# Performance work log

Measured on AMD Instinct MI355X. Metric: run time of the kernel, lower is better.

Reference implementation:

```python
import jax, jax.numpy as jnp
import numpy as np

NB_HEAD = 8
SIZE_PER_HEAD = 64
MAX_LEN = 1024
D_IN = 512
BATCH = 8
NEG_BIG = 1e12  # matches the torch module's mask * 1000000000000.0


def setup_inputs() -> dict:
    key = jax.random.key(0)
    ks = jax.random.split(key, 6)
    return {
        "Q_seq": jax.random.normal(ks[0], (BATCH, MAX_LEN, D_IN), dtype=jnp.float32),
        "K_seq": jax.random.normal(ks[1], (BATCH, MAX_LEN, D_IN), dtype=jnp.float32),
        "V_seq": jax.random.normal(ks[2], (BATCH, MAX_LEN, D_IN), dtype=jnp.float32),
        "WQ": jax.random.normal(ks[3], (D_IN, NB_HEAD * SIZE_PER_HEAD), dtype=jnp.float32),
        "WK": jax.random.normal(ks[4], (D_IN, NB_HEAD * SIZE_PER_HEAD), dtype=jnp.float32),
        "WV": jax.random.normal(ks[5], (D_IN, NB_HEAD * SIZE_PER_HEAD), dtype=jnp.float32),
    }


def reference(Q_seq, K_seq, V_seq, WQ, WK, WV):
    B, L, _ = Q_seq.shape
    H, D = NB_HEAD, SIZE_PER_HEAD
    # QKV projections -> [B, H, L, D]
    q = (Q_seq @ WQ).reshape(B, L, H, D).transpose(0, 2, 1, 3)
    k = (K_seq @ WK).reshape(B, L, H, D).transpose(0, 2, 1, 3)
    v = (V_seq @ WV).reshape(B, L, H, D).transpose(0, 2, 1, 3)
    # scaled dot-product scores [B, H, Lq, Lk]
    scores = jnp.einsum("bhqd,bhkd->bhqk", q, k) / jnp.sqrt(jnp.float32(D))
    # causal mask: the torch Mask() subtracts 1e12 where key_idx > query_idx
    causal = jnp.triu(jnp.ones((L, L), dtype=scores.dtype), k=1)  # 1 where k > q
    scores = scores - causal[None, None, :, :] * NEG_BIG
    attn = jax.nn.softmax(scores, axis=-1)
    out = jnp.einsum("bhqk,bhkd->bhqd", attn, v)  # [B, H, L, D]
    return out.transpose(0, 2, 1, 3).reshape(B, L, H * D)
```

## Files before the change

kernel.cpp:

```cpp
#include <hip/hip_runtime.h>
#include <cstddef>

#define LEN    1024
#define DIN    512
#define NHEAD  8
#define HDIM   64
#define BATCH  8

typedef __attribute__((ext_vector_type(8))) short  short8;
typedef __attribute__((ext_vector_type(4))) float  f32x4;

#define MFMA16(a, b, c) __builtin_amdgcn_mfma_f32_16x16x32_bf16((a), (b), (c), 0, 0, 0)
#define PERM_HI 0x07060302u
#define PERM_LO 0x05040100u

__device__ __forceinline__ unsigned short bf_hi(float x) {
    unsigned u = __float_as_uint(x);
    return (unsigned short)((u + 0x7fffu + ((u >> 16) & 1u)) >> 16);
}
__device__ __forceinline__ void bf_split(float x, unsigned short& h, unsigned short& l) {
    unsigned u  = __float_as_uint(x);
    unsigned hu = (u + 0x7fffu + ((u >> 16) & 1u)) >> 16;
    h = (unsigned short)hu;
    l = bf_hi(x - __uint_as_float(hu << 16));
}
__device__ __forceinline__ void unpack4(uint4 u, ushort4& h, ushort4& l) {
    h = make_ushort4((unsigned short)(u.x >> 16), (unsigned short)(u.y >> 16),
                     (unsigned short)(u.z >> 16), (unsigned short)(u.w >> 16));
    l = make_ushort4((unsigned short)(u.x & 0xffff), (unsigned short)(u.y & 0xffff),
                     (unsigned short)(u.z & 0xffff), (unsigned short)(u.w & 0xffff));
}
__device__ __forceinline__ void unpack8(uint4 a, uint4 b, uint4& h, uint4& l) {
    h = make_uint4(__builtin_amdgcn_perm(a.y, a.x, PERM_HI),
                   __builtin_amdgcn_perm(a.w, a.z, PERM_HI),
                   __builtin_amdgcn_perm(b.y, b.x, PERM_HI),
                   __builtin_amdgcn_perm(b.w, b.z, PERM_HI));
    l = make_uint4(__builtin_amdgcn_perm(a.y, a.x, PERM_LO),
                   __builtin_amdgcn_perm(a.w, a.z, PERM_LO),
                   __builtin_amdgcn_perm(b.y, b.x, PERM_LO),
                   __builtin_amdgcn_perm(b.w, b.z, PERM_LO));
}

template<int CTRL>
__device__ __forceinline__ float dpp_mov(float x) {
    return __int_as_float(__builtin_amdgcn_update_dpp(
        0, __float_as_int(x), CTRL, 0xF, 0xF, true));
}
__device__ __forceinline__ float red16_max(float x) {
    x = fmaxf(x, dpp_mov<0xB1>(x));
    x = fmaxf(x, dpp_mov<0x4E>(x));
    x = fmaxf(x, dpp_mov<0x141>(x));
    x = fmaxf(x, dpp_mov<0x140>(x));
    return x;
}
__device__ __forceinline__ float red16_sum(float x) {
    x += dpp_mov<0xB1>(x);
    x += dpp_mov<0x4E>(x);
    x += dpp_mov<0x141>(x);
    x += dpp_mov<0x140>(x);
    return x;
}

__global__ __launch_bounds__(256)
void wprep(const float* __restrict__ WQ, const float* __restrict__ WK,
           const float* __restrict__ WV, unsigned short* __restrict__ wt)
{
    __shared__ float T[64][68];
    const int z = blockIdx.z;
    const float* W = (z == 0) ? WQ : (z == 1) ? WK : WV;
    unsigned short* Wth = wt + (size_t)z * 524288;
    unsigned short* Wtl = Wth + 262144;
    const int k0 = blockIdx.x * 64, n0 = blockIdx.y * 64;
    const int t = threadIdx.x;
    #pragma unroll
    for (int e = 0; e < 4; ++e) {
        int f = e * 256 + t, r = f >> 4, c4 = (f & 15) << 2;
        *(float4*)&T[r][c4] = *(const float4*)&W[(size_t)(k0 + r) * 512 + n0 + c4];
    }
    __syncthreads();
    #pragma unroll
    for (int e = 0; e < 4; ++e) {
        int f = e * 256 + t, nr = f >> 4, kc4 = (f & 15) << 2;
        ushort4 h, l;
        bf_split(T[kc4 + 0][nr], h.x, l.x);
        bf_split(T[kc4 + 1][nr], h.y, l.y);
        bf_split(T[kc4 + 2][nr], h.z, l.z);
        bf_split(T[kc4 + 3][nr], h.w, l.w);
        *(ushort4*)&Wth[(size_t)(n0 + nr) * 512 + k0 + kc4] = h;
        *(ushort4*)&Wtl[(size_t)(n0 + nr) * 512 + k0 + kc4] = l;
    }
}

#define PSTR 40

__global__ __launch_bounds__(256)
void proj_mfma(const float* __restrict__ Qin, const float* __restrict__ Kin,
               const float* __restrict__ Vin, const unsigned short* __restrict__ wt,
               unsigned int* __restrict__ qhl, unsigned int* __restrict__ khl,
               unsigned short* __restrict__ vh)
{
    __shared__ unsigned short Ah[128 * PSTR], Al[128 * PSTR],
                              Bh[128 * PSTR], Bl[128 * PSTR];
    const int z = blockIdx.z;
    const bool full = (z < 2);
    const float* X = (z == 0) ? Qin : (z == 1) ? Kin : Vin;
    const unsigned short* Wth = wt + (size_t)z * 524288;
    const unsigned short* Wtl = Wth + 262144;

    const int t = threadIdx.x, lane = t & 63, w = t >> 6;
    const int wm = w & 1, wn = w >> 1;
    const int m0 = blockIdx.x * 128, n0 = blockIdx.y * 128;
    const int lm = lane & 15, lq = lane >> 4;
    const int ar = t >> 1, ak = (t & 1) * 16;

    const float* Xp = X + (size_t)(m0 + ar) * 512 + ak;
    const unsigned short* Bph = Wth + (size_t)(n0 + ar) * 512 + ak;
    const unsigned short* Bpl = Wtl + (size_t)(n0 + ar) * 512 + ak;

    f32x4 acc[4][4];
    #pragma unroll
    for (int i = 0; i < 4; ++i)
        #pragma unroll
        for (int j = 0; j < 4; ++j) acc[i][j] = 0.f;

    float4 av[4];
    uint4 bh0, bh1, bl0, bl1;
    #pragma unroll
    for (int e = 0; e < 4; ++e) av[e] = *(const float4*)(Xp + e * 4);
    bh0 = *(const uint4*)(Bph);
    bh1 = *(const uint4*)(Bph + 8);
    if (full) { bl0 = *(const uint4*)(Bpl); bl1 = *(const uint4*)(Bpl + 8); }

    for (int k0 = 0; k0 < 512; k0 += 32) {
        __syncthreads();
        {
            const float* ff = (const float*)&av[0];
            uint hw[16];
            #pragma unroll
            for (int i = 0; i < 16; ++i) hw[i] = __float_as_uint(ff[i]) & 0xffff0000u;
            uint4 ahv  = make_uint4(__builtin_amdgcn_perm(hw[1],  hw[0],  PERM_HI),
                                    __builtin_amdgcn_perm(hw[3],  hw[2],  PERM_HI),
                                    __builtin_amdgcn_perm(hw[5],  hw[4],  PERM_HI),
                                    __builtin_amdgcn_perm(hw[7],  hw[6],  PERM_HI));
            uint4 ahv2 = make_uint4(__builtin_amdgcn_perm(hw[9],  hw[8],  PERM_HI),
                                    __builtin_amdgcn_perm(hw[11], hw[10], PERM_HI),
                                    __builtin_amdgcn_perm(hw[13], hw[12], PERM_HI),
                                    __builtin_amdgcn_perm(hw[15], hw[14], PERM_HI));
            *(uint4*)&Ah[ar * PSTR + ak]     = ahv;
            *(uint4*)&Ah[ar * PSTR + ak + 8] = ahv2;
            if (full) {
                uint lo[8];
                #pragma unroll
                for (int i = 0; i < 8; ++i) {
                    float r0 = ff[2*i]   - __uint_as_float(hw[2*i]);
                    float r1 = ff[2*i+1] - __uint_as_float(hw[2*i+1]);
                    lo[i] = ((uint)bf_hi(r1) << 16) | bf_hi(r0);
                }
                *(uint4*)&Al[ar * PSTR + ak]     = make_uint4(lo[0], lo[1], lo[2], lo[3]);
                *(uint4*)&Al[ar * PSTR + ak + 8] = make_uint4(lo[4], lo[5], lo[6], lo[7]);
            }
        }
        *(uint4*)&Bh[ar * PSTR + ak]     = bh0;
        *(uint4*)&Bh[ar * PSTR + ak + 8] = bh1;
        if (full) {
            *(uint4*)&Bl[ar * PSTR + ak]     = bl0;
            *(uint4*)&Bl[ar * PSTR + ak + 8] = bl1;
        }
        __syncthreads();

        if (k0 + 32 < 512) {
            #pragma unroll
            for (int e = 0; e < 4; ++e) av[e] = *(const float4*)(Xp + k0 + 32 + e * 4);
            bh0 = *(const uint4*)(Bph + k0 + 32);
            bh1 = *(const uint4*)(Bph + k0 + 40);
            if (full) {
                bl0 = *(const uint4*)(Bpl + k0 + 32);
                bl1 = *(const uint4*)(Bpl + k0 + 40);
            }
        }

        short8 a_h[4], a_l[4];
        #pragma unroll
        for (int mi = 0; mi < 4; ++mi) {
            int off = (wm * 64 + mi * 16 + lm) * PSTR + lq * 8;
            a_h[mi] = *(const short8*)&Ah[off];
            if (full) a_l[mi] = *(const short8*)&Al[off];
        }
        #pragma unroll
        for (int ni = 0; ni < 4; ++ni) {
            int off = (wn * 64 + ni * 16 + lm) * PSTR + lq * 8;
            short8 b_h = *(const short8*)&Bh[off];
            if (full) {
                short8 b_l = *(const short8*)&Bl[off];
                #pragma unroll
                for (int mi = 0; mi < 4; ++mi) {
                    acc[mi][ni] = MFMA16(a_l[mi], b_h, acc[mi][ni]);
                    acc[mi][ni] = MFMA16(a_h[mi], b_l, acc[mi][ni]);
                    acc[mi][ni] = MFMA16(a_h[mi], b_h, acc[mi][ni]);
                }
            } else {
                #pragma unroll
                for (int mi = 0; mi < 4; ++mi)
                    acc[mi][ni] = MFMA16(a_h[mi], b_h, acc[mi][ni]);
            }
        }
    }

    if (z < 2) {
        unsigned int* o = (z == 0) ? qhl : khl;
        const float sc = (z == 0) ? 0.18033688011112042f : 1.0f;
        #pragma unroll
        for (int mi = 0; mi < 4; ++mi)
            #pragma unroll
            for (int ni = 0; ni < 4; ++ni) {
                int n_abs = n0 + wn * 64 + ni * 16 + lm;
                int hd = n_abs >> 6, d = n_abs & 63;
                #pragma unroll
                for (int r = 0; r < 4; ++r) {
                    int m_abs = m0 + wm * 64 + mi * 16 + lq * 4 + r;
                    int b = m_abs >> 10, li = m_abs & 1023;
                    unsigned short hv, lv;
                    bf_split(acc[mi][ni][r] * sc, hv, lv);
                    o[(((size_t)b * NHEAD + hd) * LEN + li) * HDIM + d] =
                        ((unsigned)hv << 16) | lv;
                }
            }
    } else {
        #pragma unroll
        for (int mi = 0; mi < 4; ++mi) {
            int m_base = m0 + wm * 64 + mi * 16 + lq * 4;
            int b = m_base >> 10, l0 = m_base & 1023;
            #pragma unroll
            for (int ni = 0; ni < 4; ++ni) {
                int n_abs = n0 + wn * 64 + ni * 16 + lm;
                int hd = n_abs >> 6, d = n_abs & 63;
                ushort4 hv = make_ushort4(bf_hi(acc[mi][ni][0]), bf_hi(acc[mi][ni][1]),
                                          bf_hi(acc[mi][ni][2]), bf_hi(acc[mi][ni][3]));
                *(ushort4*)&vh[(((size_t)b * NHEAD + hd) * HDIM + d) * LEN + l0] = hv;
            }
        }
    }
}

__global__ __launch_bounds__(256)
void attn_mfma(const unsigned int* __restrict__ qhl, const unsigned int* __restrict__ khl,
               const unsigned short* __restrict__ vth, float* __restrict__ out)
{
    __shared__ unsigned short sm[18432];
    unsigned short* Kh  = sm;
    unsigned short* Kl  = sm + 4608;
    unsigned short* Pb  = sm;
    unsigned short* Vt  = sm + 9216;
    unsigned short* Qsh = sm;
    unsigned short* Qsl = sm + 9216;

    const int t = threadIdx.x, lane = t & 63, w = t >> 6;
    const int lm = lane & 15, lq = lane >> 4;
    const int bx = blockIdx.x;
    const int qt = 7 - (bx >> 6);
    const int bh = bx & 63;
    const size_t base = (size_t)bh * LEN * HDIM;
    const unsigned int*   qb = qhl + base;
    const unsigned int*   kb = khl + base;
    const unsigned short* vb = vth + base;
    const int Q0  = qt * 128;
    const int Q0w = Q0 + w * 32;

    #pragma unroll
    for (int e = 0; e < 8; ++e) {
        int f = e * 256 + t, r = f >> 4, c4 = (f & 15) << 2;
        uint4 u = *(const uint4*)&qb[(size_t)(Q0 + r) * 64 + c4];
        ushort4 h, l;
        unpack4(u, h, l);
        *(ushort4*)&Qsh[r * 72 + c4] = h;
        *(ushort4*)&Qsl[r * 72 + c4] = l;
    }
    __syncthreads();
    short8 qfh[2][2], qfl[2][2];
    #pragma unroll
    for (int mi = 0; mi < 2; ++mi)
        #pragma unroll
        for (int ks = 0; ks < 2; ++ks) {
            int off = (w * 32 + mi * 16 + lm) * 72 + ks * 32 + lq * 8;
            qfh[mi][ks] = *(const short8*)&Qsh[off];
            qfl[mi][ks] = *(const short8*)&Qsl[off];
        }

    float m_i[2][4], l_i[2][4];
    f32x4 oacc[2][4];
    #pragma unroll
    for (int mi = 0; mi < 2; ++mi)
        #pragma unroll
        for (int r = 0; r < 4; ++r) { m_i[mi][r] = -1e30f; l_i[mi][r] = 0.f; }
    #pragma unroll
    for (int mi = 0; mi < 2; ++mi)
        #pragma unroll
        for (int nd = 0; nd < 4; ++nd) oacc[mi][nd] = 0.f;

    const int kr = t >> 2, kq = t & 3;
    const int vd_ = t >> 3, vs8 = (t & 7) << 3;

    uint4 kreg[4], vreg[2];
    #pragma unroll
    for (int e = 0; e < 4; ++e)
        kreg[e] = *(const uint4*)&kb[(size_t)kr * 64 + kq * 16 + e * 4];
    #pragma unroll
    for (int e = 0; e < 2; ++e)
        vreg[e] = *(const uint4*)&vb[(size_t)(e * 32 + vd_) * LEN + vs8];

    const int jend = 2 * qt + 1;
    for (int jb = 0; jb <= jend; ++jb) {
        __syncthreads();
        {
            uint4 h0, l0, h1, l1;
            unpack8(kreg[0], kreg[1], h0, l0);
            unpack8(kreg[2], kreg[3], h1, l1);
            int ko = kr * 72 + kq * 16;
            *(uint4*)&Kh[ko]     = h0;
            *(uint4*)&Kh[ko + 8] = h1;
            *(uint4*)&Kl[ko]     = l0;
            *(uint4*)&Kl[ko + 8] = l1;
            *(uint4*)&Vt[(vd_)      * 72 + vs8] = vreg[0];
            *(uint4*)&Vt[(vd_ + 32) * 72 + vs8] = vreg[1];
        }
        __syncthreads();

        if (jb < jend) {
            #pragma unroll
            for (int e = 0; e < 4; ++e)
                kreg[e] = *(const uint4*)&kb[(size_t)((jb + 1) * 64 + kr) * 64 + kq * 16 + e * 4];
            #pragma unroll
            for (int e = 0; e < 2; ++e)
                vreg[e] = *(const uint4*)&vb[(size_t)(e * 32 + vd_) * LEN + (jb + 1) * 64 + vs8];
        }

        const bool active = (jb * 64 <= Q0w + 31);
        f32x4 sf[2][4];
        if (active) {
            #pragma unroll
            for (int mi = 0; mi < 2; ++mi)
                #pragma unroll
                for (int ni = 0; ni < 4; ++ni) sf[mi][ni] = 0.f;
            #pragma unroll
            for (int ks = 0; ks < 2; ++ks)
                #pragma unroll
                for (int ni = 0; ni < 4; ++ni) {
                    int off = (ni * 16 + lm) * 72 + ks * 32 + lq * 8;
                    short8 b_h = *(const short8*)&Kh[off];
                    short8 b_l = *(const short8*)&Kl[off];
                    #pragma unroll
                    for (int mi = 0; mi < 2; ++mi) {
                        sf[mi][ni] = MFMA16(qfl[mi][ks], b_h, sf[mi][ni]);
                        sf[mi][ni] = MFMA16(qfh[mi][ks], b_l, sf[mi][ni]);
                        sf[mi][ni] = MFMA16(qfh[mi][ks], b_h, sf[mi][ni]);
                    }
                }
            if (jb * 64 + 63 > Q0w) {
                #pragma unroll
                for (int mi = 0; mi < 2; ++mi)
                    #pragma unroll
                    for (int ni = 0; ni < 4; ++ni) {
                        int key = jb * 64 + ni * 16 + lm;
                        #pragma unroll
                        for (int r = 0; r < 4; ++r) {
                            int qi = Q0w + mi * 16 + lq * 4 + r;
                            if (key > qi) sf[mi][ni][r] = -1e30f;
                        }
                    }
            }
        }
        __syncthreads();

        if (active) {
            #pragma unroll
            for (int mi = 0; mi < 2; ++mi)
                #pragma unroll
                for (int r = 0; r < 4; ++r) {
                    float mv = fmaxf(fmaxf(sf[mi][0][r], sf[mi][1][r]),
                                     fmaxf(sf[mi][2][r], sf[mi][3][r]));
                    mv = red16_max(mv);
                    float mo = m_i[mi][r];
                    float mn = fmaxf(mo, mv);
                    float al = __builtin_amdgcn_exp2f(mo - mn);
                    m_i[mi][r] = mn;
                    float rs = 0.f;
                    int prow = (w * 32 + mi * 16 + lq * 4 + r) * 72 + lm;
                    #pragma unroll
                    for (int ni = 0; ni < 4; ++ni) {
                        float p = __builtin_amdgcn_exp2f(sf[mi][ni][r] - mn);
                        rs += p;
                        Pb[prow + ni * 16] = bf_hi(p);
                    }
                    rs = red16_sum(rs);
                    l_i[mi][r] = l_i[mi][r] * al + rs;
                    #pragma unroll
                    for (int nd = 0; nd < 4; ++nd) oacc[mi][nd][r] *= al;
                }
            short8 pf[2][2];
            #pragma unroll
            for (int mi = 0; mi < 2; ++mi)
                #pragma unroll
                for (int ks = 0; ks < 2; ++ks)
                    pf[mi][ks] = *(const short8*)&Pb[(w * 32 + mi * 16 + lm) * 72 + ks * 32 + lq * 8];
            #pragma unroll
            for (int ks = 0; ks < 2; ++ks)
                #pragma unroll
                for (int nd = 0; nd < 4; ++nd) {
                    short8 vf = *(const short8*)&Vt[(nd * 16 + lm) * 72 + ks * 32 + lq * 8];
                    #pragma unroll
                    for (int mi = 0; mi < 2; ++mi)
                        oacc[mi][nd] = MFMA16(pf[mi][ks], vf, oacc[mi][nd]);
                }
        }
    }

    const int b = bh >> 3, hd = bh & 7;
    #pragma unroll
    for (int mi = 0; mi < 2; ++mi)
        #pragma unroll
        for (int r = 0; r < 4; ++r) {
            int qrow = Q0w + mi * 16 + lq * 4 + r;
            float inv = 1.0f / l_i[mi][r];
            #pragma unroll
            for (int nd = 0; nd < 4; ++nd) {
                int d = nd * 16 + lm;
                out[((size_t)b * LEN + qrow) * (NHEAD * HDIM) + hd * 64 + d] =
                    oacc[mi][nd][r] * inv;
            }
        }
}

extern "C" void kernel_launch(void* const* d_in, const int* in_sizes, int n_in,
                              void* d_out, int out_size, void* d_ws, size_t ws_size,
                              hipStream_t stream)
{
    const float* Qin = (const float*)d_in[0];
    const float* Kin = (const float*)d_in[1];
    const float* Vin = (const float*)d_in[2];
    const float* WQ  = (const float*)d_in[3];
    const float* WK  = (const float*)d_in[4];
    const float* WV  = (const float*)d_in[5];

    const size_t per = (size_t)BATCH * NHEAD * LEN * HDIM;
    unsigned int*   qhl = (unsigned int*)d_ws;
    unsigned int*   khl = qhl + per;
    unsigned short* vh  = (unsigned short*)(khl + per);
    unsigned short* wt  = vh + per;

    wprep    <<<dim3(8, 8, 3),  256, 0, stream>>>(WQ, WK, WV, wt);
    proj_mfma<<<dim3(64, 4, 3), 256, 0, stream>>>(Qin, Kin, Vin, wt, qhl, khl, vh);
    attn_mfma<<<dim3(512),      256, 0, stream>>>(qhl, khl, vh, (float*)d_out);
}
```

Before: 189.3 us.

## Load projection MFMA fragments directly from global and remap blocks per XCD

```diff
diff --git a/kernel.cpp b/kernel.cpp
--- a/kernel.cpp
+++ b/kernel.cpp
@@ -39,6 +39,9 @@
                    __builtin_amdgcn_perm(a.w, a.z, PERM_LO),
                    __builtin_amdgcn_perm(b.y, b.x, PERM_LO),
                    __builtin_amdgcn_perm(b.w, b.z, PERM_LO));
+}
+__device__ __forceinline__ short8 as_s8(uint4 u) {
+    union { uint4 u; short8 s; } x; x.u = u; return x.s;
 }
 
 template<int CTRL>
@@ -91,17 +94,19 @@
     }
 }
 
-#define PSTR 40
-
 __global__ __launch_bounds__(256)
 void proj_mfma(const float* __restrict__ Qin, const float* __restrict__ Kin,
                const float* __restrict__ Vin, const unsigned short* __restrict__ wt,
                unsigned int* __restrict__ qhl, unsigned int* __restrict__ khl,
                unsigned short* __restrict__ vh)
 {
-    __shared__ unsigned short Ah[128 * PSTR], Al[128 * PSTR],
-                              Bh[128 * PSTR], Bl[128 * PSTR];
-    const int z = blockIdx.z;
+    const int lid = blockIdx.x;
+    const int xcd = lid & 7, g = lid >> 3;
+    const int n_blk = g & 3;
+    const int uu = (g >> 2) * 8 + xcd;
+    const int z = uu >> 6;
+    const int m_blk = uu & 63;
+    const int m0 = m_blk * 128, n0 = n_blk * 128;
     const bool full = (z < 2);
     const float* X = (z == 0) ? Qin : (z == 1) ? Kin : Vin;
     const unsigned short* Wth = wt + (size_t)z * 524288;
@@ -109,13 +114,11 @@
 
     const int t = threadIdx.x, lane = t & 63, w = t >> 6;
     const int wm = w & 1, wn = w >> 1;
-    const int m0 = blockIdx.x * 128, n0 = blockIdx.y * 128;
     const int lm = lane & 15, lq = lane >> 4;
-    const int ar = t >> 1, ak = (t & 1) * 16;
-
-    const float* Xp = X + (size_t)(m0 + ar) * 512 + ak;
-    const unsigned short* Bph = Wth + (size_t)(n0 + ar) * 512 + ak;
-    const unsigned short* Bpl = Wtl + (size_t)(n0 + ar) * 512 + ak;
+
+    const float*          Ap  = X   + (size_t)(m0 + wm * 64 + lm) * 512 + lq * 8;
+    const unsigned short* Bhp = Wth + (size_t)(n0 + wn * 64 + lm) * 512 + lq * 8;
+    const unsigned short* Blp = Wtl + (size_t)(n0 + wn * 64 + lm) * 512 + lq * 8;
 
     f32x4 acc[4][4];
     #pragma unroll
@@ -123,75 +126,48 @@
         #pragma unroll
         for (int j = 0; j < 4; ++j) acc[i][j] = 0.f;
 
-    float4 av[4];
-    uint4 bh0, bh1, bl0, bl1;
-    #pragma unroll
-    for (int e = 0; e < 4; ++e) av[e] = *(const float4*)(Xp + e * 4);
-    bh0 = *(const uint4*)(Bph);
-    bh1 = *(const uint4*)(Bph + 8);
-    if (full) { bl0 = *(const uint4*)(Bpl); bl1 = *(const uint4*)(Bpl + 8); }
-
+    #pragma unroll 1
     for (int k0 = 0; k0 < 512; k0 += 32) {
-        __syncthreads();
-        {
-            const float* ff = (const float*)&av[0];
-            uint hw[16];
-            #pragma unroll
-            for (int i = 0; i < 16; ++i) hw[i] = __float_as_uint(ff[i]) & 0xffff0000u;
-            uint4 ahv  = make_uint4(__builtin_amdgcn_perm(hw[1],  hw[0],  PERM_HI),
-                                    __builtin_amdgcn_perm(hw[3],  hw[2],  PERM_HI),
-                                    __builtin_amdgcn_perm(hw[5],  hw[4],  PERM_HI),
-                                    __builtin_amdgcn_perm(hw[7],  hw[6],  PERM_HI));
-            uint4 ahv2 = make_uint4(__builtin_amdgcn_perm(hw[9],  hw[8],  PERM_HI),
-                                    __builtin_amdgcn_perm(hw[11], hw[10], PERM_HI),
-                                    __builtin_amdgcn_perm(hw[13], hw[12], PERM_HI),
-                                    __builtin_amdgcn_perm(hw[15], hw[14], PERM_HI));
-            *(uint4*)&Ah[ar * PSTR + ak]     = ahv;
-            *(uint4*)&Ah[ar * PSTR + ak + 8] = ahv2;
+        short8 a_h[4], a_l[4];
+        uint4  bh[4], bl[4];
+        #pragma unroll
+        for (int ni = 0; ni < 4; ++ni) {
+            bh[ni] = *(const uint4*)(Bhp + ni * (16 * 512) + k0);
+            if (full) bl[ni] = *(const uint4*)(Blp + ni * (16 * 512) + k0);
+        }
+        #pragma unroll
+        for (int mi = 0; mi < 4; ++mi) {
+            float4 f0 = *(const float4*)(Ap + (size_t)mi * (16 * 512) + k0);
+            float4 f1 = *(const float4*)(Ap + (size_t)mi * (16 * 512) + k0 + 4);
+            uint u0 = __float_as_uint(f0.x), u1 = __float_as_uint(f0.y),
+                 u2 = __float_as_uint(f0.z), u3 = __float_as_uint(f0.w),
+                 u4 = __float_as_uint(f1.x), u5 = __float_as_uint(f1.y),
+                 u6 = __float_as_uint(f1.z), u7 = __float_as_uint(f1.w);
+            a_h[mi] = as_s8(make_uint4(__builtin_amdgcn_perm(u1, u0, PERM_HI),
+                                       __builtin_amdgcn_perm(u3, u2, PERM_HI),
+                                       __builtin_amdgcn_perm(u5, u4, PERM_HI),
+                                       __builtin_amdgcn_perm(u7, u6, PERM_HI)));
             if (full) {
-                uint lo[8];
-                #pragma unroll
-                for (int i = 0; i < 8; ++i) {
-                    float r0 = ff[2*i]   - __uint_as_float(hw[2*i]);
-                    float r1 = ff[2*i+1] - __uint_as_float(hw[2*i+1]);
-                    lo[i] = ((uint)bf_hi(r1) << 16) | bf_hi(r0);
-                }
-                *(uint4*)&Al[ar * PSTR + ak]     = make_uint4(lo[0], lo[1], lo[2], lo[3]);
-                *(uint4*)&Al[ar * PSTR + ak + 8] = make_uint4(lo[4], lo[5], lo[6], lo[7]);
-            }
-        }
-        *(uint4*)&Bh[ar * PSTR + ak]     = bh0;
-        *(uint4*)&Bh[ar * PSTR + ak + 8] = bh1;
-        if (full) {
-            *(uint4*)&Bl[ar * PSTR + ak]     = bl0;
-            *(uint4*)&Bl[ar * PSTR + ak + 8] = bl1;
-        }
-        __syncthreads();
-
-        if (k0 + 32 < 512) {
-            #pragma unroll
-            for (int e = 0; e < 4; ++e) av[e] = *(const float4*)(Xp + k0 + 32 + e * 4);
-            bh0 = *(const uint4*)(Bph + k0 + 32);
-            bh1 = *(const uint4*)(Bph + k0 + 40);
+                float r0 = f0.x - __uint_as_float(u0 & 0xffff0000u);
+                float r1 = f0.y - __uint_as_float(u1 & 0xffff0000u);
+                float r2 = f0.z - __uint_as_float(u2 & 0xffff0000u);
+                float r3 = f0.w - __uint_as_float(u3 & 0xffff0000u);
+                float r4 = f1.x - __uint_as_float(u4 & 0xffff0000u);
+                float r5 = f1.y - __uint_as_float(u5 & 0xffff0000u);
+                float r6 = f1.z - __uint_as_float(u6 & 0xffff0000u);
+                float r7 = f1.w - __uint_as_float(u7 & 0xffff0000u);
+                a_l[mi] = as_s8(make_uint4(
+                    __builtin_amdgcn_perm(__float_as_uint(r1), __float_as_uint(r0), PERM_HI),
+                    __builtin_amdgcn_perm(__float_as_uint(r3), __float_as_uint(r2), PERM_HI),
+                    __builtin_amdgcn_perm(__float_as_uint(r5), __float_as_uint(r4), PERM_HI),
+                    __builtin_amdgcn_perm(__float_as_uint(r7), __float_as_uint(r6), PERM_HI)));
+            }
+        }
+        #pragma unroll
+        for (int ni = 0; ni < 4; ++ni) {
+            short8 b_h = as_s8(bh[ni]);
             if (full) {
-                bl0 = *(const uint4*)(Bpl + k0 + 32);
-                bl1 = *(const uint4*)(Bpl + k0 + 40);
-            }
-        }
-
-        short8 a_h[4], a_l[4];
-        #pragma unroll
-        for (int mi = 0; mi < 4; ++mi) {
-            int off = (wm * 64 + mi * 16 + lm) * PSTR + lq * 8;
-            a_h[mi] = *(const short8*)&Ah[off];
-            if (full) a_l[mi] = *(const short8*)&Al[off];
-        }
-        #pragma unroll
-        for (int ni = 0; ni < 4; ++ni) {
-            int off = (wn * 64 + ni * 16 + lm) * PSTR + lq * 8;
-            short8 b_h = *(const short8*)&Bh[off];
-            if (full) {
-                short8 b_l = *(const short8*)&Bl[off];
+                short8 b_l = as_s8(bl[ni]);
                 #pragma unroll
                 for (int mi = 0; mi < 4; ++mi) {
                     acc[mi][ni] = MFMA16(a_l[mi], b_h, acc[mi][ni]);
@@ -447,7 +423,7 @@
     unsigned short* vh  = (unsigned short*)(khl + per);
     unsigned short* wt  = vh + per;
 
-    wprep    <<<dim3(8, 8, 3),  256, 0, stream>>>(WQ, WK, WV, wt);
-    proj_mfma<<<dim3(64, 4, 3), 256, 0, stream>>>(Qin, Kin, Vin, wt, qhl, khl, vh);
-    attn_mfma<<<dim3(512),      256, 0, stream>>>(qhl, khl, vh, (float*)d_out);
-}
+    wprep    <<<dim3(8, 8, 3), 256, 0, stream>>>(WQ, WK, WV, wt);
+    proj_mfma<<<dim3(768),     256, 0, stream>>>(Qin, Kin, Vin, wt, qhl, khl, vh);
+    attn_mfma<<<dim3(512),     256, 0, stream>>>(qhl, khl, vh, (float*)d_out);
+}
```

New measurement: 250.2 us. 1.32x slower.
